# Optimization experiments

Hardware: AMD Instinct MI355X
Metric: run time of the kernel (lower is better)

The kernel has to match this reference:

```python
import jax, jax.numpy as jnp
import numpy as np

B, N, L, C = 16, 2048, 12, 32  # batch, num_nodes, seq_len, channels


def setup_inputs() -> dict:
    key = jax.random.key(0)
    k1, k2, k3 = jax.random.split(key, 3)
    x = jax.random.normal(k1, (B, N, L, C), dtype=jnp.float32)
    # memory parameter: xavier_uniform over (channels, num_nodes)
    limit = float(np.sqrt(6.0 / (C + N)))
    memory = jax.random.uniform(k2, (C, N), minval=-limit, maxval=limit, dtype=jnp.float32)
    # nn.Linear(2, 1): weight (1, 2), bias (1,)
    fc_limit = float(np.sqrt(1.0 / 2.0))
    fc_w = jax.random.uniform(k3, (1, 2), minval=-fc_limit, maxval=fc_limit, dtype=jnp.float32)
    fc_b = jnp.zeros((1,), dtype=jnp.float32)
    return {"x": x, "memory": memory, "fc_w": fc_w, "fc_b": fc_b}


def reference(x, memory, fc_w, fc_b):
    # x: (B, N, L, C) -> permute to (B, C, N, L) as in the torch module
    xp = jnp.transpose(x, (0, 3, 1, 2))
    scale = 1.0 / float(np.sqrt(xp.shape[1]))  # 1/sqrt(channels)
    # adj_dyn_1: einsum over channel+time with memory -> (B, N, N)
    a1 = jax.nn.softmax(jax.nn.relu(jnp.einsum('bcnl,cm->bnm', xp, memory) * scale), axis=-1)
    # adj_dyn_2: time-summed node features gram matrix -> (B, N, N)
    xs = xp.sum(-1)  # (B, C, N)
    a2 = jax.nn.softmax(jax.nn.relu(jnp.einsum('bcn,bcm->bnm', xs, xs) * scale), axis=-1)
    # fc over the stacked pair: Linear(2,1) == w0*a1 + w1*a2 + b
    adj = a1 * fc_w[0, 0] + a2 * fc_w[0, 1] + fc_b[0]  # (B, N, N)
    k = int(adj.shape[1] * 0.8)
    _, idx = jax.lax.top_k(adj, k)  # idx: (B, N, k)
    b_ix = jnp.arange(adj.shape[0])[:, None, None]
    n_ix = jnp.arange(adj.shape[1])[None, :, None]
    mask = jnp.zeros_like(adj).at[b_ix, n_ix, idx].set(1.0)
    return jax.nn.softmax(adj * mask, axis=-1)
```

## Files before the change

### kernel.cpp

```cpp
#include <hip/hip_runtime.h>
#include <hip/hip_bf16.h>
#include <cstdint>
#include <cstddef>

#define B_ 16
#define N_ 2048
#define L_ 12
#define C_ 32
#define KTOP 1638
#define SCALE 0.17677669529663687f
#define LOG2E 1.44269504088896f

typedef __attribute__((ext_vector_type(8))) short short8v;
typedef __attribute__((ext_vector_type(4))) float f32x4;

#if __has_builtin(__builtin_amdgcn_exp2f)
#define EXP2F(x) __builtin_amdgcn_exp2f(x)
#else
#define EXP2F(x) exp2f(x)
#endif

__device__ __forceinline__ unsigned short bf16_rne(float v) {
  unsigned u = __float_as_uint(v);
  u += 0x7FFFu + ((u >> 16) & 1u);
  return (unsigned short)(u >> 16);
}

__global__ __launch_bounds__(256) void prep_kernel(const float* __restrict__ x,
                                                   const float* __restrict__ mem,
                                                   unsigned short* __restrict__ xsH,
                                                   unsigned short* __restrict__ xsL,
                                                   unsigned short* __restrict__ memT) {
  const int b = blockIdx.y, n0 = blockIdx.x * 64;
  const int c = threadIdx.x & 31, nr = threadIdx.x >> 5;
#pragma unroll
  for (int i = 0; i < 8; ++i) {
    const int n = n0 + i * 8 + nr;
    const float* px = x + ((size_t)(b * N_ + n) * L_) * C_ + c;
    float s = 0.f;
#pragma unroll
    for (int l = 0; l < L_; ++l) s += px[l * C_];
    const unsigned short h = bf16_rne(s);
    const float hf = __uint_as_float((unsigned)h << 16);
    const unsigned short lo = bf16_rne(s - hf);
    const size_t o = (size_t)(b * N_ + n) * C_ + c;
    xsH[o] = h;
    xsL[o] = lo;
  }
  if (b == 0) {
#pragma unroll
    for (int i = 0; i < 8; ++i) {
      const int idx = i * 256 + threadIdx.x;
      const int ml = idx >> 5, cc = idx & 31;
      memT[(size_t)(n0 + ml) * C_ + cc] = bf16_rne(mem[(size_t)cc * N_ + n0 + ml]);
    }
  }
}

__global__ __launch_bounds__(512, 4) void adj_kernel(
    const unsigned short* __restrict__ xsH, const unsigned short* __restrict__ xsL,
    const unsigned short* __restrict__ memT, const float* __restrict__ fc_w,
    const float* __restrict__ fc_b, float* __restrict__ out) {
  __shared__ unsigned pbuf[8][2049];
  __shared__ float red1[8][8], red2[8][8];

  const int tid = threadIdx.x, wid = tid >> 6, lane = tid & 63;
  const int l15 = lane & 15, g = lane >> 4;
  const int b = blockIdx.y, n0 = blockIdx.x * 8;

  const int fr = (l15 < 8) ? l15 : ((l15 - 6) & 7);
  const size_t arow = (size_t)(b * N_ + n0 + fr) * C_ + g * 8;
  const short8v hiA = *(const short8v*)(xsH + arow);
  const short8v loA = *(const short8v*)(xsL + arow);

  const f32x4 zero = {0.f, 0.f, 0.f, 0.f};
  float s1[2] = {0.f, 0.f}, s2[2] = {0.f, 0.f};
  const float K = SCALE * LOG2E;
  const float C2 = -80.f * LOG2E;
  const int g8 = g * 8;
  const int rbase = (g & 1) * 4 + (g & 2);
  const int mbase = wid * 256 + l15;
  const size_t bcol = (size_t)b * N_ * C_ + (size_t)mbase * C_ + g8;
  const unsigned short* pH = xsH + bcol;
  const unsigned short* pL = xsL + bcol;
  const unsigned short* pM = memT + (size_t)mbase * C_ + g8;
  unsigned* pw = &pbuf[rbase][mbase];

#pragma unroll
  for (int t = 0; t < 16; ++t) {
    const short8v hiB = *(const short8v*)(pH + t * (16 * C_));
    const short8v loB = *(const short8v*)(pL + t * (16 * C_));
    const short8v mB  = *(const short8v*)(pM + t * (16 * C_));

    f32x4 acc1 = __builtin_amdgcn_mfma_f32_16x16x32_bf16(hiA, mB, zero, 0, 0, 0);
    f32x4 acc2 = __builtin_amdgcn_mfma_f32_16x16x32_bf16(hiA, hiB, zero, 0, 0, 0);
    acc2 = __builtin_amdgcn_mfma_f32_16x16x32_bf16(hiA, loB, acc2, 0, 0, 0);
    acc2 = __builtin_amdgcn_mfma_f32_16x16x32_bf16(loA, hiB, acc2, 0, 0, 0);

#pragma unroll
    for (int s = 0; s < 2; ++s) {
      const float p1 = EXP2F(fmaxf(acc1[s], 0.f) * K);
      const float p2 = EXP2F(fminf(fmaf(fmaxf(acc2[s], 0.f), K, C2), 127.f));
      s1[s] += p1;
      s2[s] += p2;
      union { __hip_bfloat162 h2; unsigned u; } pk;
      pk.h2 = __float22bfloat162_rn(float2{p1, p2});
      pw[s * 2049 + t * 16] = pk.u;
    }
  }

#pragma unroll
  for (int d = 1; d < 16; d <<= 1) {
#pragma unroll
    for (int s = 0; s < 2; ++s) {
      s1[s] += __shfl_xor(s1[s], d);
      s2[s] += __shfl_xor(s2[s], d);
    }
  }
  if (l15 == 0) {
#pragma unroll
    for (int s = 0; s < 2; ++s) {
      red1[wid][rbase + s] = s1[s];
      red2[wid][rbase + s] = s2[s];
    }
  }
  __syncthreads();

  {
    const int r = wid;
    float S1 = 0.f, S2 = 0.f;
#pragma unroll
    for (int w = 0; w < 8; ++w) { S1 += red1[w][r]; S2 += red2[w][r]; }
    const float w0 = fc_w[0], w1 = fc_w[1], bb = fc_b[0];
    const float i1 = w0 / S1, i2 = w1 / S2;
    const unsigned* prow = &pbuf[0][0] + r * 2049;

    unsigned pk[16];
    unsigned kg[16];
#pragma unroll
    for (int j = 0; j < 16; ++j) {
      const unsigned qa = prow[lane + (2 * j) * 64];
      const unsigned qb = prow[lane + (2 * j + 1) * 64];
      const float adjA = fmaf(__uint_as_float(qa & 0xFFFF0000u), i2,
                        fmaf(__uint_as_float(qa << 16), i1, bb));
      const float adjB = fmaf(__uint_as_float(qb & 0xFFFF0000u), i2,
                        fmaf(__uint_as_float(qb << 16), i1, bb));
      union { __hip_bfloat162 h2; unsigned u; } c;
      c.h2 = __float22bfloat162_rn(float2{adjA, adjB});
      pk[j] = c.u;
      const unsigned sgn = (c.u >> 15) & 0x00010001u;
      const unsigned srt = c.u ^ 0x80008000u ^ (sgn * 0x7FFFu);
      kg[j] = ((srt >> 1) & 0x7FFF7FFFu) | 0x80008000u;
    }

    const float p2t = __uint_as_float((unsigned)bf16_rne(EXP2F(C2)) << 16);
    const float Tval = fmaf(p2t, i2, fmaf(1.0f, i1, bb));
    const unsigned short bT = bf16_rne(Tval);
    const unsigned sT = bT >> 15;
    const unsigned kT = ((((unsigned)bT ^ 0x8000u ^ (sT * 0x7FFFu)) >> 1) & 0x7FFFu);

    const unsigned mmA = kT * 0x10001u;
    const unsigned mmB = (kT + 1u) * 0x10001u;
    unsigned cAp = 0, cBp = 0;
#pragma unroll
    for (int j = 0; j < 16; ++j) {
      cAp += ((kg[j] - mmA) >> 15) & 0x10001u;
      cBp += ((kg[j] - mmB) >> 15) & 0x10001u;
    }
    unsigned comb = ((cAp & 0xFFFFu) + (cAp >> 16)) |
                    (((cBp & 0xFFFFu) + (cBp >> 16)) << 16);
#pragma unroll
    for (int d = 1; d < 64; d <<= 1) comb += (unsigned)__shfl_xor((int)comb, d);
    const unsigned cge = comb & 0xFFFFu, cgt = comb >> 16;

    unsigned lo;
    if (cge >= KTOP && cgt < KTOP) {
      lo = kT;
    } else {
      unsigned mnv = 0xFFFFu, mxv = 0u;
#pragma unroll
      for (int j = 0; j < 16; ++j) {
        const unsigned k15 = kg[j] & 0x7FFF7FFFu;
        mnv = min(mnv, min(k15 & 0xFFFFu, k15 >> 16));
        mxv = max(mxv, max(k15 & 0xFFFFu, k15 >> 16));
      }
#pragma unroll
      for (int d = 1; d < 64; d <<= 1) {
        mnv = min(mnv, (unsigned)__shfl_xor((int)mnv, d));
        mxv = max(mxv, (unsigned)__shfl_xor((int)mxv, d));
      }
      unsigned hi;
      if (cge < KTOP) { lo = mnv; hi = kT - 1u; }
      else            { lo = kT + 1u; hi = mxv; }
#pragma unroll 1
      for (int it = 0; it < 15; ++it) {
        if (lo >= hi) break;
        const unsigned mid = (lo + hi + 1u) >> 1;
        const unsigned mm = mid * 0x10001u;
        unsigned c0 = 0;
#pragma unroll
        for (int j = 0; j < 16; ++j) c0 += ((kg[j] - mm) >> 15) & 0x10001u;
        unsigned cnt = (c0 & 0xFFFFu) + (c0 >> 16);
#pragma unroll
        for (int d = 1; d < 64; d <<= 1) cnt += (unsigned)__shfl_xor((int)cnt, d);
        if (cnt >= KTOP) lo = mid; else hi = mid - 1u;
      }
    }

    const unsigned lolo = lo * 0x10001u;
    float ex[32];
    float s = 0.f;
#pragma unroll
    for (int j = 0; j < 16; ++j) {
      const unsigned ge = kg[j] - lolo;
      float eA = EXP2F(__uint_as_float(pk[j] << 16) * LOG2E);
      float eB = EXP2F(__uint_as_float(pk[j] & 0xFFFF0000u) * LOG2E);
      eA = (ge & 0x8000u) ? eA : 1.0f;
      eB = (ge & 0x80000000u) ? eB : 1.0f;
      ex[2 * j] = eA; ex[2 * j + 1] = eB;
      s += eA + eB;
    }
#pragma unroll
    for (int d = 1; d < 64; d <<= 1) s += __shfl_xor(s, d);
    const float inv = 1.f / s;
    float* op = out + ((size_t)b * N_ + n0 + r) * N_;
#pragma unroll
    for (int j = 0; j < 32; ++j) op[lane + (j << 6)] = ex[j] * inv;
  }
}

extern "C" void kernel_launch(void* const* d_in, const int* in_sizes, int n_in,
                              void* d_out, int out_size, void* d_ws, size_t ws_size,
                              hipStream_t stream) {
  const float* x   = (const float*)d_in[0];
  const float* mem = (const float*)d_in[1];
  const float* fcw = (const float*)d_in[2];
  const float* fcb = (const float*)d_in[3];
  float* out = (float*)d_out;
  unsigned short* xsH  = (unsigned short*)d_ws;
  unsigned short* xsL  = xsH + (size_t)B_ * N_ * C_;
  unsigned short* memT = xsL + (size_t)B_ * N_ * C_;

  dim3 g1(N_ / 64, B_);
  prep_kernel<<<g1, 256, 0, stream>>>(x, mem, xsH, xsL, memT);
  dim3 g2(N_ / 8, B_);
  adj_kernel<<<g2, 512, 0, stream>>>(xsH, xsL, memT, fcw, fcb, out);
}
```

Measured before the change: 146.6 us.

## Keep adjacency tiles in registers and use 1024-thread blocks with cross-wave reductions

The block grows to 16 waves, each computing 128 columns for all 8 rows. The packed exp values now stay in registers instead of a 64 KB shared-memory staging buffer, which also removes the transpose back through LDS. Row sums, the top-k threshold counts, the binary-search fallback and the softmax sum are now reduced across waves through small shared arrays and extra barriers. The intent is to cut LDS traffic and the occupancy limit that buffer imposed. In exchange, output stores become 64-byte segments per row instead of fully contiguous 256-byte wave stores, and the rare fallback search needs two barriers per iteration.

```diff
diff --git a/kernel.cpp b/kernel.cpp
--- a/kernel.cpp
+++ b/kernel.cpp
@@ -10,6 +10,7 @@
 #define KTOP 1638
 #define SCALE 0.17677669529663687f
 #define LOG2E 1.44269504088896f
+#define TS 8
 
 typedef __attribute__((ext_vector_type(8))) short short8v;
 typedef __attribute__((ext_vector_type(4))) float f32x4;
@@ -24,6 +25,10 @@
   unsigned u = __float_as_uint(v);
   u += 0x7FFFu + ((u >> 16) & 1u);
   return (unsigned short)(u >> 16);
+}
+__device__ __forceinline__ unsigned key15(unsigned short b16) {
+  const unsigned s = b16 >> 15;
+  return ((((unsigned)b16) ^ 0x8000u ^ (s * 0x7FFFu)) >> 1) & 0x7FFFu;
 }
 
 __global__ __launch_bounds__(256) void prep_kernel(const float* __restrict__ x,
@@ -57,37 +62,39 @@
   }
 }
 
-__global__ __launch_bounds__(512, 4) void adj_kernel(
+__global__ __launch_bounds__(1024) void adj_kernel(
     const unsigned short* __restrict__ xsH, const unsigned short* __restrict__ xsL,
     const unsigned short* __restrict__ memT, const float* __restrict__ fc_w,
     const float* __restrict__ fc_b, float* __restrict__ out) {
-  __shared__ unsigned pbuf[8][2049];
-  __shared__ float red1[8][8], red2[8][8];
+  __shared__ float redS1[8][16], redS2[8][16];
+  __shared__ unsigned redC[2][4][16];
+  __shared__ float redE[8][16];
 
   const int tid = threadIdx.x, wid = tid >> 6, lane = tid & 63;
   const int l15 = lane & 15, g = lane >> 4;
   const int b = blockIdx.y, n0 = blockIdx.x * 8;
 
   const int fr = (l15 < 8) ? l15 : ((l15 - 6) & 7);
-  const size_t arow = (size_t)(b * N_ + n0 + fr) * C_ + g * 8;
+  const int rbase = (g & 1) * 4 + (g & 2);
+  const int g8 = g * 8;
+  const size_t arow = (size_t)(b * N_ + n0 + fr) * C_ + g8;
   const short8v hiA = *(const short8v*)(xsH + arow);
-  const short8v loA = *(const short8v*)(xsL + arow);
+  const short8v loFA = *(const short8v*)(xsL + arow);
 
   const f32x4 zero = {0.f, 0.f, 0.f, 0.f};
-  float s1[2] = {0.f, 0.f}, s2[2] = {0.f, 0.f};
   const float K = SCALE * LOG2E;
   const float C2 = -80.f * LOG2E;
-  const int g8 = g * 8;
-  const int rbase = (g & 1) * 4 + (g & 2);
-  const int mbase = wid * 256 + l15;
+  const int mbase = wid * 128 + l15;
   const size_t bcol = (size_t)b * N_ * C_ + (size_t)mbase * C_ + g8;
   const unsigned short* pH = xsH + bcol;
   const unsigned short* pL = xsL + bcol;
   const unsigned short* pM = memT + (size_t)mbase * C_ + g8;
-  unsigned* pw = &pbuf[rbase][mbase];
-
-#pragma unroll
-  for (int t = 0; t < 16; ++t) {
+
+  float s1[2] = {0.f, 0.f}, s2[2] = {0.f, 0.f};
+  unsigned pA[TS], pB[TS];
+
+#pragma unroll
+  for (int t = 0; t < TS; ++t) {
     const short8v hiB = *(const short8v*)(pH + t * (16 * C_));
     const short8v loB = *(const short8v*)(pL + t * (16 * C_));
     const short8v mB  = *(const short8v*)(pM + t * (16 * C_));
@@ -95,17 +102,23 @@
     f32x4 acc1 = __builtin_amdgcn_mfma_f32_16x16x32_bf16(hiA, mB, zero, 0, 0, 0);
     f32x4 acc2 = __builtin_amdgcn_mfma_f32_16x16x32_bf16(hiA, hiB, zero, 0, 0, 0);
     acc2 = __builtin_amdgcn_mfma_f32_16x16x32_bf16(hiA, loB, acc2, 0, 0, 0);
-    acc2 = __builtin_amdgcn_mfma_f32_16x16x32_bf16(loA, hiB, acc2, 0, 0, 0);
-
-#pragma unroll
-    for (int s = 0; s < 2; ++s) {
-      const float p1 = EXP2F(fmaxf(acc1[s], 0.f) * K);
-      const float p2 = EXP2F(fminf(fmaf(fmaxf(acc2[s], 0.f), K, C2), 127.f));
-      s1[s] += p1;
-      s2[s] += p2;
+    acc2 = __builtin_amdgcn_mfma_f32_16x16x32_bf16(loFA, hiB, acc2, 0, 0, 0);
+
+    {
+      const float p1 = EXP2F(fmaxf(acc1[0], 0.f) * K);
+      const float p2 = EXP2F(fminf(fmaf(fmaxf(acc2[0], 0.f), K, C2), 127.f));
+      s1[0] += p1; s2[0] += p2;
       union { __hip_bfloat162 h2; unsigned u; } pk;
       pk.h2 = __float22bfloat162_rn(float2{p1, p2});
-      pw[s * 2049 + t * 16] = pk.u;
+      pA[t] = pk.u;
+    }
+    {
+      const float p1 = EXP2F(fmaxf(acc1[1], 0.f) * K);
+      const float p2 = EXP2F(fminf(fmaf(fmaxf(acc2[1], 0.f), K, C2), 127.f));
+      s1[1] += p1; s2[1] += p2;
+      union { __hip_bfloat162 h2; unsigned u; } pk;
+      pk.h2 = __float22bfloat162_rn(float2{p1, p2});
+      pB[t] = pk.u;
     }
   }
 
@@ -118,114 +131,144 @@
     }
   }
   if (l15 == 0) {
-#pragma unroll
-    for (int s = 0; s < 2; ++s) {
-      red1[wid][rbase + s] = s1[s];
-      red2[wid][rbase + s] = s2[s];
-    }
+    redS1[rbase][wid] = s1[0]; redS1[rbase + 1][wid] = s1[1];
+    redS2[rbase][wid] = s2[0]; redS2[rbase + 1][wid] = s2[1];
   }
   __syncthreads();
-
-  {
-    const int r = wid;
-    float S1 = 0.f, S2 = 0.f;
-#pragma unroll
-    for (int w = 0; w < 8; ++w) { S1 += red1[w][r]; S2 += red2[w][r]; }
-    const float w0 = fc_w[0], w1 = fc_w[1], bb = fc_b[0];
-    const float i1 = w0 / S1, i2 = w1 / S2;
-    const unsigned* prow = &pbuf[0][0] + r * 2049;
-
-    unsigned pk[16];
-    unsigned kg[16];
-#pragma unroll
-    for (int j = 0; j < 16; ++j) {
-      const unsigned qa = prow[lane + (2 * j) * 64];
-      const unsigned qb = prow[lane + (2 * j + 1) * 64];
-      const float adjA = fmaf(__uint_as_float(qa & 0xFFFF0000u), i2,
-                        fmaf(__uint_as_float(qa << 16), i1, bb));
-      const float adjB = fmaf(__uint_as_float(qb & 0xFFFF0000u), i2,
-                        fmaf(__uint_as_float(qb << 16), i1, bb));
-      union { __hip_bfloat162 h2; unsigned u; } c;
-      c.h2 = __float22bfloat162_rn(float2{adjA, adjB});
-      pk[j] = c.u;
-      const unsigned sgn = (c.u >> 15) & 0x00010001u;
-      const unsigned srt = c.u ^ 0x80008000u ^ (sgn * 0x7FFFu);
-      kg[j] = ((srt >> 1) & 0x7FFF7FFFu) | 0x80008000u;
-    }
-
-    const float p2t = __uint_as_float((unsigned)bf16_rne(EXP2F(C2)) << 16);
-    const float Tval = fmaf(p2t, i2, fmaf(1.0f, i1, bb));
-    const unsigned short bT = bf16_rne(Tval);
-    const unsigned sT = bT >> 15;
-    const unsigned kT = ((((unsigned)bT ^ 0x8000u ^ (sT * 0x7FFFu)) >> 1) & 0x7FFFu);
-
-    const unsigned mmA = kT * 0x10001u;
-    const unsigned mmB = (kT + 1u) * 0x10001u;
-    unsigned cAp = 0, cBp = 0;
-#pragma unroll
-    for (int j = 0; j < 16; ++j) {
-      cAp += ((kg[j] - mmA) >> 15) & 0x10001u;
-      cBp += ((kg[j] - mmB) >> 15) & 0x10001u;
-    }
-    unsigned comb = ((cAp & 0xFFFFu) + (cAp >> 16)) |
-                    (((cBp & 0xFFFFu) + (cBp >> 16)) << 16);
-#pragma unroll
-    for (int d = 1; d < 64; d <<= 1) comb += (unsigned)__shfl_xor((int)comb, d);
-    const unsigned cge = comb & 0xFFFFu, cgt = comb >> 16;
-
-    unsigned lo;
-    if (cge >= KTOP && cgt < KTOP) {
-      lo = kT;
-    } else {
-      unsigned mnv = 0xFFFFu, mxv = 0u;
-#pragma unroll
-      for (int j = 0; j < 16; ++j) {
-        const unsigned k15 = kg[j] & 0x7FFF7FFFu;
-        mnv = min(mnv, min(k15 & 0xFFFFu, k15 >> 16));
-        mxv = max(mxv, max(k15 & 0xFFFFu, k15 >> 16));
-      }
-#pragma unroll
-      for (int d = 1; d < 64; d <<= 1) {
-        mnv = min(mnv, (unsigned)__shfl_xor((int)mnv, d));
-        mxv = max(mxv, (unsigned)__shfl_xor((int)mxv, d));
-      }
-      unsigned hi;
-      if (cge < KTOP) { lo = mnv; hi = kT - 1u; }
-      else            { lo = kT + 1u; hi = mxv; }
+  float S1A = 0.f, S1B = 0.f, S2A = 0.f, S2B = 0.f;
+#pragma unroll
+  for (int w = 0; w < 16; ++w) {
+    S1A += redS1[rbase][w]; S1B += redS1[rbase + 1][w];
+    S2A += redS2[rbase][w]; S2B += redS2[rbase + 1][w];
+  }
+  const float w0 = fc_w[0], w1 = fc_w[1], bb = fc_b[0];
+  const float i1A = w0 / S1A, i2A = w1 / S2A;
+  const float i1B = w0 / S1B, i2B = w1 / S2B;
+
+  unsigned kg[TS], mk[TS];
+#pragma unroll
+  for (int t = 0; t < TS; ++t) {
+    const unsigned qa = pA[t], qb = pB[t];
+    const float adjA = fmaf(__uint_as_float(qa & 0xFFFF0000u), i2A,
+                      fmaf(__uint_as_float(qa << 16), i1A, bb));
+    const float adjB = fmaf(__uint_as_float(qb & 0xFFFF0000u), i2B,
+                      fmaf(__uint_as_float(qb << 16), i1B, bb));
+    union { __hip_bfloat162 h2; unsigned u; } c;
+    c.h2 = __float22bfloat162_rn(float2{adjA, adjB});
+    mk[t] = c.u;
+    const unsigned sgn = (c.u >> 15) & 0x00010001u;
+    const unsigned srt = c.u ^ 0x80008000u ^ (sgn * 0x7FFFu);
+    kg[t] = ((srt >> 1) & 0x7FFF7FFFu) | 0x80008000u;
+  }
+
+  const float p2t = __uint_as_float((unsigned)bf16_rne(EXP2F(C2)) << 16);
+  const unsigned kTA = key15(bf16_rne(fmaf(p2t, i2A, fmaf(1.0f, i1A, bb))));
+  const unsigned kTB = key15(bf16_rne(fmaf(p2t, i2B, fmaf(1.0f, i1B, bb))));
+  const unsigned mmA = kTA | (kTB << 16);
+  const unsigned mmB = (kTA + 1u) | ((kTB + 1u) << 16);
+  unsigned cge = 0, cgt = 0;
+#pragma unroll
+  for (int t = 0; t < TS; ++t) {
+    cge += ((kg[t] - mmA) >> 15) & 0x10001u;
+    cgt += ((kg[t] - mmB) >> 15) & 0x10001u;
+  }
+#pragma unroll
+  for (int d = 1; d < 16; d <<= 1) {
+    cge += (unsigned)__shfl_xor((int)cge, d);
+    cgt += (unsigned)__shfl_xor((int)cgt, d);
+  }
+  if (l15 == 0) { redC[0][g][wid] = cge; redC[1][g][wid] = cgt; }
+  __syncthreads();
+  unsigned CGE = 0, CGT = 0;
+#pragma unroll
+  for (int w = 0; w < 16; ++w) { CGE += redC[0][g][w]; CGT += redC[1][g][w]; }
+  const unsigned cgeA = CGE & 0xFFFFu, cgeB = CGE >> 16;
+  const unsigned cgtA = CGT & 0xFFFFu, cgtB = CGT >> 16;
+  const bool okA = (cgeA >= KTOP) && (cgtA < KTOP);
+  const bool okB = (cgeB >= KTOP) && (cgtB < KTOP);
+  unsigned thrA = kTA, thrB = kTB;
+
+  if (!__all(okA && okB)) {
+    __syncthreads();
+    unsigned mnA = 0x7FFFu, mxA = 0u, mnB = 0x7FFFu, mxB = 0u;
+#pragma unroll
+    for (int t = 0; t < TS; ++t) {
+      const unsigned kA = kg[t] & 0x7FFFu, kB = (kg[t] >> 16) & 0x7FFFu;
+      mnA = min(mnA, kA); mxA = max(mxA, kA);
+      mnB = min(mnB, kB); mxB = max(mxB, kB);
+    }
+#pragma unroll
+    for (int d = 1; d < 16; d <<= 1) {
+      mnA = min(mnA, (unsigned)__shfl_xor((int)mnA, d));
+      mxA = max(mxA, (unsigned)__shfl_xor((int)mxA, d));
+      mnB = min(mnB, (unsigned)__shfl_xor((int)mnB, d));
+      mxB = max(mxB, (unsigned)__shfl_xor((int)mxB, d));
+    }
+    if (l15 == 0) {
+      redC[0][g][wid] = mnA | (mnB << 16);
+      redC[1][g][wid] = mxA | (mxB << 16);
+    }
+    __syncthreads();
+    mnA = 0x7FFFu; mxA = 0u; mnB = 0x7FFFu; mxB = 0u;
+#pragma unroll
+    for (int w = 0; w < 16; ++w) {
+      const unsigned vn = redC[0][g][w], vx = redC[1][g][w];
+      mnA = min(mnA, vn & 0xFFFFu); mnB = min(mnB, vn >> 16);
+      mxA = max(mxA, vx & 0xFFFFu); mxB = max(mxB, vx >> 16);
+    }
+    unsigned lA = mnA, hA = mxA, lB = mnB, hB = mxB;
 #pragma unroll 1
-      for (int it = 0; it < 15; ++it) {
-        if (lo >= hi) break;
-        const unsigned mid = (lo + hi + 1u) >> 1;
-        const unsigned mm = mid * 0x10001u;
-        unsigned c0 = 0;
-#pragma unroll
-        for (int j = 0; j < 16; ++j) c0 += ((kg[j] - mm) >> 15) & 0x10001u;
-        unsigned cnt = (c0 & 0xFFFFu) + (c0 >> 16);
-#pragma unroll
-        for (int d = 1; d < 64; d <<= 1) cnt += (unsigned)__shfl_xor((int)cnt, d);
-        if (cnt >= KTOP) lo = mid; else hi = mid - 1u;
-      }
-    }
-
-    const unsigned lolo = lo * 0x10001u;
-    float ex[32];
-    float s = 0.f;
-#pragma unroll
-    for (int j = 0; j < 16; ++j) {
-      const unsigned ge = kg[j] - lolo;
-      float eA = EXP2F(__uint_as_float(pk[j] << 16) * LOG2E);
-      float eB = EXP2F(__uint_as_float(pk[j] & 0xFFFF0000u) * LOG2E);
-      eA = (ge & 0x8000u) ? eA : 1.0f;
-      eB = (ge & 0x80000000u) ? eB : 1.0f;
-      ex[2 * j] = eA; ex[2 * j + 1] = eB;
-      s += eA + eB;
-    }
-#pragma unroll
-    for (int d = 1; d < 64; d <<= 1) s += __shfl_xor(s, d);
-    const float inv = 1.f / s;
-    float* op = out + ((size_t)b * N_ + n0 + r) * N_;
-#pragma unroll
-    for (int j = 0; j < 32; ++j) op[lane + (j << 6)] = ex[j] * inv;
+    for (int it = 0; it < 15; ++it) {
+      const unsigned midA = (lA + hA + 1u) >> 1;
+      const unsigned midB = (lB + hB + 1u) >> 1;
+      const unsigned mm = midA | (midB << 16);
+      unsigned cnt = 0;
+#pragma unroll
+      for (int t = 0; t < TS; ++t) cnt += ((kg[t] - mm) >> 15) & 0x10001u;
+#pragma unroll
+      for (int d = 1; d < 16; d <<= 1) cnt += (unsigned)__shfl_xor((int)cnt, d);
+      __syncthreads();
+      if (l15 == 0) redC[0][g][wid] = cnt;
+      __syncthreads();
+      unsigned CNT = 0;
+#pragma unroll
+      for (int w = 0; w < 16; ++w) CNT += redC[0][g][w];
+      const unsigned cA = CNT & 0xFFFFu, cB = CNT >> 16;
+      if (cA >= KTOP) lA = midA; else hA = midA - 1u;
+      if (cB >= KTOP) lB = midB; else hB = midB - 1u;
+    }
+    thrA = lA; thrB = lB;
+  }
+
+  const unsigned lolo = thrA | (thrB << 16);
+  float sA = 0.f, sB = 0.f;
+#pragma unroll
+  for (int t = 0; t < TS; ++t) {
+    const unsigned ge = kg[t] - lolo;
+    const unsigned msk = ((ge & 0x8000u) ? 0xFFFFu : 0u) |
+                         ((ge & 0x80000000u) ? 0xFFFF0000u : 0u);
+    mk[t] &= msk;
+    sA += EXP2F(__uint_as_float(mk[t] << 16) * LOG2E);
+    sB += EXP2F(__uint_as_float(mk[t] & 0xFFFF0000u) * LOG2E);
+  }
+#pragma unroll
+  for (int d = 1; d < 16; d <<= 1) {
+    sA += __shfl_xor(sA, d);
+    sB += __shfl_xor(sB, d);
+  }
+  if (l15 == 0) { redE[rbase][wid] = sA; redE[rbase + 1][wid] = sB; }
+  __syncthreads();
+  float SEA = 0.f, SEB = 0.f;
+#pragma unroll
+  for (int w = 0; w < 16; ++w) { SEA += redE[rbase][w]; SEB += redE[rbase + 1][w]; }
+  const float invA = 1.f / SEA, invB = 1.f / SEB;
+
+  float* opA = out + ((size_t)(b * N_ + n0 + rbase)) * N_ + mbase;
+  float* opB = opA + N_;
+#pragma unroll
+  for (int t = 0; t < TS; ++t) {
+    opA[t * 16] = EXP2F(__uint_as_float(mk[t] << 16) * LOG2E) * invA;
+    opB[t * 16] = EXP2F(__uint_as_float(mk[t] & 0xFFFF0000u) * LOG2E) * invB;
   }
 }
 
@@ -244,5 +287,5 @@
   dim3 g1(N_ / 64, B_);
   prep_kernel<<<g1, 256, 0, stream>>>(x, mem, xsH, xsL, memT);
   dim3 g2(N_ / 8, B_);
-  adj_kernel<<<g2, 512, 0, stream>>>(xsH, xsL, memT, fcw, fcb, out);
-}
+  adj_kernel<<<g2, 1024, 0, stream>>>(xsH, xsL, memT, fcw, fcb, out);
+}
```

Result: slower. 227.8 us (+55.4%).

## Shrink LDS staging with uint8/bf16 split, raise occupancy, vectorize stores, polynomial exp

Applied to the files above, without the earlier changes.

The packed bf16x2 staging buffer is split into a uint8 quantized buffer for the first softmax numerator (p1 in [1, ~3]) and a bf16 buffer for the second. This shrinks LDS per block so occupancy can rise, and launch bounds move from 4 to 6 blocks. The epilogue now reads 4 contiguous columns per lane and writes float4 stores. It uses a cubic Taylor approximation of exp, falling back to the hardware exp2 when any lane sees |a| > 0.25. It also recomputes exps in the store loop instead of holding 32 floats live. The 8-bit quantization of p1 and the polynomial exp add approximation error that relies on the adjacency values being small.

```diff
diff --git a/kernel.cpp b/kernel.cpp
--- a/kernel.cpp
+++ b/kernel.cpp
@@ -25,6 +25,10 @@
   u += 0x7FFFu + ((u >> 16) & 1u);
   return (unsigned short)(u >> 16);
 }
+__device__ __forceinline__ unsigned key15(unsigned short b16) {
+  const unsigned s = b16 >> 15;
+  return ((((unsigned)b16) ^ 0x8000u ^ (s * 0x7FFFu)) >> 1) & 0x7FFFu;
+}
 
 __global__ __launch_bounds__(256) void prep_kernel(const float* __restrict__ x,
                                                    const float* __restrict__ mem,
@@ -57,11 +61,12 @@
   }
 }
 
-__global__ __launch_bounds__(512, 4) void adj_kernel(
+__global__ __launch_bounds__(512, 6) void adj_kernel(
     const unsigned short* __restrict__ xsH, const unsigned short* __restrict__ xsL,
     const unsigned short* __restrict__ memT, const float* __restrict__ fc_w,
     const float* __restrict__ fc_b, float* __restrict__ out) {
-  __shared__ unsigned pbuf[8][2049];
+  __shared__ unsigned char  p1b[8][2080];
+  __shared__ unsigned short p2b[8][2064];
   __shared__ float red1[8][8], red2[8][8];
 
   const int tid = threadIdx.x, wid = tid >> 6, lane = tid & 63;
@@ -69,24 +74,24 @@
   const int b = blockIdx.y, n0 = blockIdx.x * 8;
 
   const int fr = (l15 < 8) ? l15 : ((l15 - 6) & 7);
-  const size_t arow = (size_t)(b * N_ + n0 + fr) * C_ + g * 8;
+  const int rbase = (g & 1) * 4 + (g & 2);
+  const int g8 = g * 8;
+  const size_t arow = (size_t)(b * N_ + n0 + fr) * C_ + g8;
   const short8v hiA = *(const short8v*)(xsH + arow);
-  const short8v loA = *(const short8v*)(xsL + arow);
+  const short8v loFA = *(const short8v*)(xsL + arow);
 
   const f32x4 zero = {0.f, 0.f, 0.f, 0.f};
-  float s1[2] = {0.f, 0.f}, s2[2] = {0.f, 0.f};
   const float K = SCALE * LOG2E;
   const float C2 = -80.f * LOG2E;
-  const int g8 = g * 8;
-  const int rbase = (g & 1) * 4 + (g & 2);
   const int mbase = wid * 256 + l15;
   const size_t bcol = (size_t)b * N_ * C_ + (size_t)mbase * C_ + g8;
   const unsigned short* pH = xsH + bcol;
   const unsigned short* pL = xsL + bcol;
   const unsigned short* pM = memT + (size_t)mbase * C_ + g8;
-  unsigned* pw = &pbuf[rbase][mbase];
-
-#pragma unroll
+
+  float s1[2] = {0.f, 0.f}, s2[2] = {0.f, 0.f};
+
+#pragma unroll 2
   for (int t = 0; t < 16; ++t) {
     const short8v hiB = *(const short8v*)(pH + t * (16 * C_));
     const short8v loB = *(const short8v*)(pL + t * (16 * C_));
@@ -95,17 +100,16 @@
     f32x4 acc1 = __builtin_amdgcn_mfma_f32_16x16x32_bf16(hiA, mB, zero, 0, 0, 0);
     f32x4 acc2 = __builtin_amdgcn_mfma_f32_16x16x32_bf16(hiA, hiB, zero, 0, 0, 0);
     acc2 = __builtin_amdgcn_mfma_f32_16x16x32_bf16(hiA, loB, acc2, 0, 0, 0);
-    acc2 = __builtin_amdgcn_mfma_f32_16x16x32_bf16(loA, hiB, acc2, 0, 0, 0);
-
+    acc2 = __builtin_amdgcn_mfma_f32_16x16x32_bf16(loFA, hiB, acc2, 0, 0, 0);
+
+    const int m = mbase + t * 16;
 #pragma unroll
     for (int s = 0; s < 2; ++s) {
       const float p1 = EXP2F(fmaxf(acc1[s], 0.f) * K);
       const float p2 = EXP2F(fminf(fmaf(fmaxf(acc2[s], 0.f), K, C2), 127.f));
-      s1[s] += p1;
-      s2[s] += p2;
-      union { __hip_bfloat162 h2; unsigned u; } pk;
-      pk.h2 = __float22bfloat162_rn(float2{p1, p2});
-      pw[s * 2049 + t * 16] = pk.u;
+      s1[s] += p1; s2[s] += p2;
+      p1b[rbase + s][m] = (unsigned char)fminf(fmaf(p1, 128.f, -127.5f), 255.f);
+      p2b[rbase + s][m] = bf16_rne(p2);
     }
   }
 
@@ -126,106 +130,130 @@
   }
   __syncthreads();
 
-  {
-    const int r = wid;
-    float S1 = 0.f, S2 = 0.f;
-#pragma unroll
-    for (int w = 0; w < 8; ++w) { S1 += red1[w][r]; S2 += red2[w][r]; }
-    const float w0 = fc_w[0], w1 = fc_w[1], bb = fc_b[0];
-    const float i1 = w0 / S1, i2 = w1 / S2;
-    const unsigned* prow = &pbuf[0][0] + r * 2049;
-
-    unsigned pk[16];
-    unsigned kg[16];
+  const int r = wid;
+  float S1 = 0.f, S2 = 0.f;
+#pragma unroll
+  for (int w = 0; w < 8; ++w) { S1 += red1[w][r]; S2 += red2[w][r]; }
+  const float w0 = fc_w[0], w1 = fc_w[1], bb = fc_b[0];
+  const float i1 = w0 / S1, i2 = w1 / S2;
+
+  unsigned pk[16], kg[16];
+  const unsigned char*  pr1 = &p1b[r][0];
+  const unsigned short* pr2 = &p2b[r][0];
+#pragma unroll
+  for (int k = 0; k < 8; ++k) {
+    const int c0 = 4 * lane + 256 * k;
+    const unsigned q8 = *(const unsigned*)(pr1 + c0);
+    const ushort4 q16 = *(const ushort4*)(pr2 + c0);
+    const float a0 = fmaf(__uint_as_float((unsigned)q16.x << 16), i2,
+                    fmaf(fmaf((float)(unsigned char)(q8      ), 0.0078125f, 1.f), i1, bb));
+    const float a1 = fmaf(__uint_as_float((unsigned)q16.y << 16), i2,
+                    fmaf(fmaf((float)(unsigned char)(q8 >>  8), 0.0078125f, 1.f), i1, bb));
+    const float a2 = fmaf(__uint_as_float((unsigned)q16.z << 16), i2,
+                    fmaf(fmaf((float)(unsigned char)(q8 >> 16), 0.0078125f, 1.f), i1, bb));
+    const float a3 = fmaf(__uint_as_float((unsigned)q16.w << 16), i2,
+                    fmaf(fmaf((float)(unsigned char)(q8 >> 24), 0.0078125f, 1.f), i1, bb));
+    union { __hip_bfloat162 h2; unsigned u; } cA, cB;
+    cA.h2 = __float22bfloat162_rn(float2{a0, a1});
+    cB.h2 = __float22bfloat162_rn(float2{a2, a3});
+    pk[2 * k] = cA.u; pk[2 * k + 1] = cB.u;
+    unsigned sgn = (cA.u >> 15) & 0x00010001u;
+    unsigned srt = cA.u ^ 0x80008000u ^ (sgn * 0x7FFFu);
+    kg[2 * k] = ((srt >> 1) & 0x7FFF7FFFu) | 0x80008000u;
+    sgn = (cB.u >> 15) & 0x00010001u;
+    srt = cB.u ^ 0x80008000u ^ (sgn * 0x7FFFu);
+    kg[2 * k + 1] = ((srt >> 1) & 0x7FFF7FFFu) | 0x80008000u;
+  }
+
+  const float p2t = __uint_as_float((unsigned)bf16_rne(EXP2F(C2)) << 16);
+  const unsigned kT = key15(bf16_rne(fmaf(p2t, i2, fmaf(1.0f, i1, bb))));
+  const unsigned mmA = kT * 0x10001u;
+  const unsigned mmB = (kT + 1u) * 0x10001u;
+  unsigned cge = 0, cgt = 0;
+#pragma unroll
+  for (int j = 0; j < 16; ++j) {
+    cge += ((kg[j] - mmA) >> 15) & 0x10001u;
+    cgt += ((kg[j] - mmB) >> 15) & 0x10001u;
+  }
+  unsigned comb = ((cge & 0xFFFFu) + (cge >> 16)) |
+                  (((cgt & 0xFFFFu) + (cgt >> 16)) << 16);
+#pragma unroll
+  for (int d = 1; d < 64; d <<= 1) comb += (unsigned)__shfl_xor((int)comb, d);
+  const unsigned nge = comb & 0xFFFFu, ngt = comb >> 16;
+  unsigned thr = kT;
+  if (!(nge >= KTOP && ngt < KTOP)) {
+    unsigned mn = 0x7FFFu, mx = 0u;
 #pragma unroll
     for (int j = 0; j < 16; ++j) {
-      const unsigned qa = prow[lane + (2 * j) * 64];
-      const unsigned qb = prow[lane + (2 * j + 1) * 64];
-      const float adjA = fmaf(__uint_as_float(qa & 0xFFFF0000u), i2,
-                        fmaf(__uint_as_float(qa << 16), i1, bb));
-      const float adjB = fmaf(__uint_as_float(qb & 0xFFFF0000u), i2,
-                        fmaf(__uint_as_float(qb << 16), i1, bb));
-      union { __hip_bfloat162 h2; unsigned u; } c;
-      c.h2 = __float22bfloat162_rn(float2{adjA, adjB});
-      pk[j] = c.u;
-      const unsigned sgn = (c.u >> 15) & 0x00010001u;
-      const unsigned srt = c.u ^ 0x80008000u ^ (sgn * 0x7FFFu);
-      kg[j] = ((srt >> 1) & 0x7FFF7FFFu) | 0x80008000u;
-    }
-
-    const float p2t = __uint_as_float((unsigned)bf16_rne(EXP2F(C2)) << 16);
-    const float Tval = fmaf(p2t, i2, fmaf(1.0f, i1, bb));
-    const unsigned short bT = bf16_rne(Tval);
-    const unsigned sT = bT >> 15;
-    const unsigned kT = ((((unsigned)bT ^ 0x8000u ^ (sT * 0x7FFFu)) >> 1) & 0x7FFFu);
-
-    const unsigned mmA = kT * 0x10001u;
-    const unsigned mmB = (kT + 1u) * 0x10001u;
-    unsigned cAp = 0, cBp = 0;
-#pragma unroll
-    for (int j = 0; j < 16; ++j) {
-      cAp += ((kg[j] - mmA) >> 15) & 0x10001u;
-      cBp += ((kg[j] - mmB) >> 15) & 0x10001u;
-    }
-    unsigned comb = ((cAp & 0xFFFFu) + (cAp >> 16)) |
-                    (((cBp & 0xFFFFu) + (cBp >> 16)) << 16);
-#pragma unroll
-    for (int d = 1; d < 64; d <<= 1) comb += (unsigned)__shfl_xor((int)comb, d);
-    const unsigned cge = comb & 0xFFFFu, cgt = comb >> 16;
-
-    unsigned lo;
-    if (cge >= KTOP && cgt < KTOP) {
-      lo = kT;
-    } else {
-      unsigned mnv = 0xFFFFu, mxv = 0u;
-#pragma unroll
-      for (int j = 0; j < 16; ++j) {
-        const unsigned k15 = kg[j] & 0x7FFF7FFFu;
-        mnv = min(mnv, min(k15 & 0xFFFFu, k15 >> 16));
-        mxv = max(mxv, max(k15 & 0xFFFFu, k15 >> 16));
+      const unsigned k15 = kg[j] & 0x7FFF7FFFu;
+      mn = min(mn, min(k15 & 0xFFFFu, k15 >> 16));
+      mx = max(mx, max(k15 & 0xFFFFu, k15 >> 16));
+    }
+#pragma unroll
+    for (int d = 1; d < 64; d <<= 1) {
+      mn = min(mn, (unsigned)__shfl_xor((int)mn, d));
+      mx = max(mx, (unsigned)__shfl_xor((int)mx, d));
+    }
+    unsigned lo2, hi2;
+    if (nge < KTOP) { lo2 = mn; hi2 = kT - 1u; } else { lo2 = kT + 1u; hi2 = mx; }
+#pragma unroll 1
+    for (int it = 0; it < 15; ++it) {
+      if (lo2 >= hi2) break;
+      const unsigned mid = (lo2 + hi2 + 1u) >> 1;
+      const unsigned mm = mid * 0x10001u;
+      unsigned c0 = 0;
+#pragma unroll
+      for (int j = 0; j < 16; ++j) c0 += ((kg[j] - mm) >> 15) & 0x10001u;
+      unsigned cnt = (c0 & 0xFFFFu) + (c0 >> 16);
+#pragma unroll
+      for (int d = 1; d < 64; d <<= 1) cnt += (unsigned)__shfl_xor((int)cnt, d);
+      if (cnt >= KTOP) lo2 = mid; else hi2 = mid - 1u;
+    }
+    thr = lo2;
+  }
+
+  const unsigned lolo = thr * 0x10001u;
+  float ssum = 0.f;
+#pragma unroll
+  for (int j = 0; j < 16; ++j) {
+    const unsigned ge = kg[j] - lolo;
+    const unsigned msk = ((ge & 0x8000u) ? 0xFFFFu : 0u) |
+                         ((ge & 0x80000000u) ? 0xFFFF0000u : 0u);
+    pk[j] &= msk;
+    const float aA = __uint_as_float(pk[j] << 16);
+    const float aB = __uint_as_float(pk[j] & 0xFFFF0000u);
+    float eA = fmaf(aA, fmaf(aA, fmaf(aA, 0.166666667f, 0.5f), 1.f), 1.f);
+    float eB = fmaf(aB, fmaf(aB, fmaf(aB, 0.166666667f, 0.5f), 1.f), 1.f);
+    if (__ballot(fmaxf(__builtin_fabsf(aA), __builtin_fabsf(aB)) > 0.25f)) {
+      eA = EXP2F(aA * LOG2E);
+      eB = EXP2F(aB * LOG2E);
+    }
+    ssum += eA + eB;
+  }
+#pragma unroll
+  for (int d = 1; d < 64; d <<= 1) ssum += __shfl_xor(ssum, d);
+  const float inv = 1.f / ssum;
+
+  float* op = out + ((size_t)(b * N_ + n0 + r)) * N_;
+#pragma unroll
+  for (int k = 0; k < 8; ++k) {
+    float e4[4];
+#pragma unroll
+    for (int h = 0; h < 2; ++h) {
+      const unsigned pj = pk[2 * k + h];
+      const float aA = __uint_as_float(pj << 16);
+      const float aB = __uint_as_float(pj & 0xFFFF0000u);
+      float eA = fmaf(aA, fmaf(aA, fmaf(aA, 0.166666667f, 0.5f), 1.f), 1.f);
+      float eB = fmaf(aB, fmaf(aB, fmaf(aB, 0.166666667f, 0.5f), 1.f), 1.f);
+      if (__ballot(fmaxf(__builtin_fabsf(aA), __builtin_fabsf(aB)) > 0.25f)) {
+        eA = EXP2F(aA * LOG2E);
+        eB = EXP2F(aB * LOG2E);
       }
-#pragma unroll
-      for (int d = 1; d < 64; d <<= 1) {
-        mnv = min(mnv, (unsigned)__shfl_xor((int)mnv, d));
-        mxv = max(mxv, (unsigned)__shfl_xor((int)mxv, d));
-      }
-      unsigned hi;
-      if (cge < KTOP) { lo = mnv; hi = kT - 1u; }
-      else            { lo = kT + 1u; hi = mxv; }
-#pragma unroll 1
-      for (int it = 0; it < 15; ++it) {
-        if (lo >= hi) break;
-        const unsigned mid = (lo + hi + 1u) >> 1;
-        const unsigned mm = mid * 0x10001u;
-        unsigned c0 = 0;
-#pragma unroll
-        for (int j = 0; j < 16; ++j) c0 += ((kg[j] - mm) >> 15) & 0x10001u;
-        unsigned cnt = (c0 & 0xFFFFu) + (c0 >> 16);
-#pragma unroll
-        for (int d = 1; d < 64; d <<= 1) cnt += (unsigned)__shfl_xor((int)cnt, d);
-        if (cnt >= KTOP) lo = mid; else hi = mid - 1u;
-      }
-    }
-
-    const unsigned lolo = lo * 0x10001u;
-    float ex[32];
-    float s = 0.f;
-#pragma unroll
-    for (int j = 0; j < 16; ++j) {
-      const unsigned ge = kg[j] - lolo;
-      float eA = EXP2F(__uint_as_float(pk[j] << 16) * LOG2E);
-      float eB = EXP2F(__uint_as_float(pk[j] & 0xFFFF0000u) * LOG2E);
-      eA = (ge & 0x8000u) ? eA : 1.0f;
-      eB = (ge & 0x80000000u) ? eB : 1.0f;
-      ex[2 * j] = eA; ex[2 * j + 1] = eB;
-      s += eA + eB;
-    }
-#pragma unroll
-    for (int d = 1; d < 64; d <<= 1) s += __shfl_xor(s, d);
-    const float inv = 1.f / s;
-    float* op = out + ((size_t)b * N_ + n0 + r) * N_;
-#pragma unroll
-    for (int j = 0; j < 32; ++j) op[lane + (j << 6)] = ex[j] * inv;
+      e4[2 * h] = eA; e4[2 * h + 1] = eB;
+    }
+    float4 o;
+    o.x = e4[0] * inv; o.y = e4[1] * inv; o.z = e4[2] * inv; o.w = e4[3] * inv;
+    *(float4*)(op + 4 * lane + 256 * k) = o;
   }
 }
 
```

Result: slower. 161.6 us (+10.3%).
